# Optimization experiments

Hardware: AMD Instinct MI355X
Metric: run time of the kernel (lower is better)

The kernel has to match this reference:

```python
import jax, jax.numpy as jnp
import numpy as np

B, SEG, DIM = 8, 16, 1024  # H = W = D = SEG is forced by the Linear(dim, dim) on H*S etc.
HID = DIM // 4


def setup_inputs() -> dict:
    key = jax.random.key(0)
    ks = jax.random.split(key, 16)
    def lin(k, i, o):
        return jax.random.normal(k, (i, o), jnp.float32) * 0.02
    return {
        "x": jax.random.normal(ks[0], (B, SEG, SEG, SEG, DIM), jnp.float32),
        "wh": lin(ks[1], DIM, DIM), "bh": jnp.zeros((DIM,), jnp.float32),
        "ww": lin(ks[2], DIM, DIM), "bw": jnp.zeros((DIM,), jnp.float32),
        "wd": lin(ks[3], DIM, DIM), "bd": jnp.zeros((DIM,), jnp.float32),
        "wc": lin(ks[4], DIM, DIM), "bc": jnp.zeros((DIM,), jnp.float32),
        "w1": lin(ks[5], DIM, HID), "b1": jnp.zeros((HID,), jnp.float32),
        "w2": lin(ks[6], HID, 4 * DIM), "b2": jnp.zeros((4 * DIM,), jnp.float32),
        "wp": lin(ks[7], DIM, DIM), "bp": jnp.zeros((DIM,), jnp.float32),
    }


def reference(x, wh, bh, ww, bw, wd, bd, wc, bc, w1, b1, w2, b2, wp, bp):
    Bn, H, Wn, D, C = x.shape
    seg = SEG
    S = C // seg
    xr = x.reshape(Bn, H, Wn, D, seg, S)

    # h-branch: mix along H axis (H*S == C)
    h = xr.transpose(0, 4, 2, 3, 1, 5).reshape(Bn, seg, Wn, D, H * S)
    h = (h @ wh + bh).reshape(Bn, seg, Wn, D, H, S).transpose(0, 4, 2, 3, 1, 5).reshape(Bn, H, Wn, D, C)

    # w-branch: mix along W axis
    w = xr.transpose(0, 1, 4, 3, 2, 5).reshape(Bn, H, seg, D, Wn * S)
    w = (w @ ww + bw).reshape(Bn, H, seg, D, Wn, S).transpose(0, 1, 4, 3, 2, 5).reshape(Bn, H, Wn, D, C)

    # d-branch: mix along D axis
    d = xr.transpose(0, 1, 2, 4, 3, 5).reshape(Bn, H, Wn, seg, D * S)
    d = (d @ wd + bd).reshape(Bn, H, Wn, seg, D, S).transpose(0, 1, 2, 4, 3, 5).reshape(Bn, H, Wn, D, C)

    # c-branch: plain channel mixing
    c = x @ wc + bc

    # reweight gate: global-average-pool then small MLP -> softmax over the 4 branches
    a = (h + w + d + c).mean(axis=(1, 2, 3))                 # (B, C)
    a = jax.nn.gelu(a @ w1 + b1, approximate=False) @ w2 + b2  # (B, 4C)
    a = jax.nn.softmax(a.reshape(Bn, C, 4).transpose(2, 0, 1), axis=0)  # (4, B, C)
    a = a[:, :, None, None, None, :]                          # (4, B, 1, 1, 1, C)

    out = h * a[0] + w * a[1] + d * a[2] + c * a[3]
    return out @ wp + bp
```

## Files before the change

### kernel.cpp

```cpp
#include <hip/hip_runtime.h>
#include <cstdint>
#include <cstddef>

typedef unsigned short u16;
typedef __attribute__((ext_vector_type(8))) __bf16 bf16x8;
typedef __attribute__((ext_vector_type(4))) float f32x4;
typedef __attribute__((ext_vector_type(4))) unsigned int u32x4;

__device__ __forceinline__ float bf2f(u16 u){
  union { unsigned int i; float f; } x; x.i = ((unsigned int)u) << 16; return x.f;
}
__device__ __forceinline__ u16 f2bf(float f){
  union { float f; unsigned int i; } x; x.f = f;
  unsigned int i = x.i;
  return (u16)((i + 0x7fffu + ((i >> 16) & 1u)) >> 16);
}
__device__ __forceinline__ void load_lds16(const u16* g, u16* l){
  __builtin_amdgcn_global_load_lds((const __attribute__((address_space(1))) void*)g,
                                   (__attribute__((address_space(3))) void*)l, 16, 0, 0);
}

__global__ __launch_bounds__(256) void k_transpose(
    const float* __restrict__ wh, const float* __restrict__ ww,
    const float* __restrict__ wd, const float* __restrict__ wc,
    const float* __restrict__ wp, u16* __restrict__ wT)
{
  __shared__ u16 tile[32][33];
  const float* src = (blockIdx.z==0)?wh:(blockIdx.z==1)?ww:(blockIdx.z==2)?wd:(blockIdx.z==3)?wc:wp;
  u16* dst = wT + (size_t)blockIdx.z * 1048576;
  int x = blockIdx.x*32 + threadIdx.x;
  int y0 = blockIdx.y*32;
  for (int i = threadIdx.y; i < 32; i += 8)
    tile[i][threadIdx.x] = f2bf(src[(size_t)(y0+i)*1024 + x]);
  __syncthreads();
  int x2 = y0 + threadIdx.x;
  int y2 = blockIdx.x*32;
  for (int i = threadIdx.y; i < 32; i += 8)
    dst[(size_t)(y2+i)*1024 + x2] = tile[threadIdx.x][i];
}

__global__ __launch_bounds__(256) void k_psum(
    const float* __restrict__ x, u16* __restrict__ xbf, float* __restrict__ P_h,
    float* __restrict__ PwP, float* __restrict__ PdP)
{
  const int b = blockIdx.x, cs = blockIdx.y, hg = blockIdx.z;
  const int th = threadIdx.x >> 7, tc = threadIdx.x & 127;
  const int h = hg*2 + th, c = cs*128 + tc;
  const size_t base = ((size_t)b<<22) + ((size_t)h<<18) + c;
  const float* xb = x + base;
  u16* xo = xbf + base;
  float sh = 0.f;
  float aW[16] = {}, aD[16] = {};
#pragma unroll
  for (int w = 0; w < 16; ++w)
#pragma unroll
    for (int d = 0; d < 16; ++d){
      float v = xb[(w<<14) + (d<<10)];
      xo[(w<<14) + (d<<10)] = f2bf(v);
      sh += v; aW[w] += v; aD[d] += v;
    }
  P_h[(size_t)((b<<4)+h)*1024 + c] = sh;
  const int part = hg*2 + th;
  float* pw = PwP + ((size_t)part<<17) + ((size_t)b<<14) + c;
  float* pd = PdP + ((size_t)part<<17) + ((size_t)b<<14) + c;
#pragma unroll
  for (int w = 0; w < 16; ++w) pw[w<<10] = aW[w];
#pragma unroll
  for (int d = 0; d < 16; ++d) pd[d<<10] = aD[d];
}

__global__ __launch_bounds__(256) void k_psum2(
    const float* __restrict__ PwP, const float* __restrict__ PdP,
    float* __restrict__ P_w, float* __restrict__ P_d)
{
  int idx = blockIdx.x*256 + threadIdx.x;
  float s = 0.f, t = 0.f;
#pragma unroll
  for (int p = 0; p < 16; ++p){ s += PwP[(size_t)p*131072 + idx]; t += PdP[(size_t)p*131072 + idx]; }
  P_w[idx] = s; P_d[idx] = t;
}

__global__ __launch_bounds__(256) void k_wred(
    const float* __restrict__ wh, const float* __restrict__ ww, const float* __restrict__ wd,
    float* __restrict__ wred)
{
  const float* src = (blockIdx.y==0)?wh:(blockIdx.y==1)?ww:wd;
  int idx = blockIdx.x*256 + threadIdx.x;
  int k = idx >> 6, S = idx & 63;
  float s = 0.f;
#pragma unroll
  for (int i = 0; i < 16; ++i) s += src[(size_t)k*1024 + i*64 + S];
  wred[(size_t)blockIdx.y*65536 + idx] = s;
}

__global__ __launch_bounds__(256) void k_asum(
    const float* __restrict__ P_h, const float* __restrict__ P_w, const float* __restrict__ P_d,
    const float* __restrict__ wred, const float* __restrict__ wc,
    const float* __restrict__ bhv, const float* __restrict__ bwv,
    const float* __restrict__ bdv, const float* __restrict__ bcv,
    float* __restrict__ a_sum)
{
  const int b = blockIdx.x, cs = blockIdx.y, tid = threadIdx.x;
  const int tc = tid & 127, ti = tid >> 7;
  const int c = cs*128 + tc, sg = c >> 6, S = c & 63;
  __shared__ float xbar[1024];
  __shared__ float red[2][128];
  for (int k = tid; k < 1024; k += 256){
    float s = 0.f;
#pragma unroll
    for (int hh = 0; hh < 16; ++hh) s += P_h[(size_t)(b*16+hh)*1024 + k];
    xbar[k] = s;
  }
  __syncthreads();
  const float* Ph = P_h + (size_t)b*16384;
  const float* Pw = P_w + (size_t)b*16384;
  const float* Pd = P_d + (size_t)b*16384;
  const float* whr = wred, *wwr = wred + 65536, *wdr = wred + 131072;
  float acc = 0.f;
  for (int i = ti*8; i < ti*8 + 8; ++i){
#pragma unroll 8
    for (int si = 0; si < 64; ++si){
      int k = i*64 + si;
      acc += Ph[i*1024 + sg*64 + si] * whr[(size_t)k*64 + S]
           + Pw[i*1024 + sg*64 + si] * wwr[(size_t)k*64 + S]
           + Pd[i*1024 + sg*64 + si] * wdr[(size_t)k*64 + S];
    }
  }
#pragma unroll 8
  for (int k = ti*512; k < ti*512 + 512; ++k) acc += xbar[k] * wc[(size_t)k*1024 + c];
  red[ti][tc] = acc;
  __syncthreads();
  if (ti == 0){
    float bs = 0.f;
#pragma unroll
    for (int i = 0; i < 16; ++i) bs += bhv[i*64+S] + bwv[i*64+S] + bdv[i*64+S];
    a_sum[b*1024 + c] = red[0][tc] + red[1][tc] + 4096.f*bcv[c] + 256.f*bs;
  }
}

__global__ __launch_bounds__(256) void k_mlp1(
    const float* __restrict__ a_sum, const float* __restrict__ w1,
    const float* __restrict__ b1, float* __restrict__ z1g)
{
  const int b = blockIdx.x, tid = threadIdx.x;
  __shared__ float af[1024];
  for (int i = tid; i < 1024; i += 256) af[i] = a_sum[b*1024 + i] * (1.0f/4096.0f);
  __syncthreads();
  float acc = b1[tid];
#pragma unroll 8
  for (int k = 0; k < 1024; ++k) acc += af[k] * w1[(size_t)k*256 + tid];
  z1g[b*256 + tid] = 0.5f * acc * (1.0f + erff(acc * 0.70710678118654752f));
}

__global__ __launch_bounds__(128) void k_mlp2(
    const float* __restrict__ z1g, const float* __restrict__ w2,
    const float* __restrict__ b2, float* __restrict__ alpha)
{
  const int b = blockIdx.x, js = blockIdx.y, tid = threadIdx.x;
  __shared__ float z1[256];
  z1[tid] = z1g[b*256 + tid];
  z1[tid+128] = z1g[b*256 + tid + 128];
  __syncthreads();
  const int cch = js*128 + tid;
  const int j0 = cch*4;
  f32x4 acc = *(const f32x4*)(b2 + j0);
#pragma unroll 8
  for (int k = 0; k < 256; ++k){
    f32x4 wv4 = *(const f32x4*)(w2 + (size_t)k*4096 + j0);
    float z = z1[k];
    acc[0] += z*wv4[0]; acc[1] += z*wv4[1]; acc[2] += z*wv4[2]; acc[3] += z*wv4[3];
  }
  float m = fmaxf(fmaxf(acc[0], acc[1]), fmaxf(acc[2], acc[3]));
  float e0 = expf(acc[0]-m), e1 = expf(acc[1]-m), e2 = expf(acc[2]-m), e3 = expf(acc[3]-m);
  float inv = 1.0f / (e0+e1+e2+e3);
  alpha[0*8192 + b*1024 + cch] = e0*inv;
  alpha[1*8192 + b*1024 + cch] = e1*inv;
  alpha[2*8192 + b*1024 + cch] = e2*inv;
  alpha[3*8192 + b*1024 + cch] = e3*inv;
}


#define STAGE_A(buf, kk, kt) \
  load_lds16(gA0 + (size_t)(kt)*strideK + (kk)*32, sA + (buf)*16384 + (kk)*8192); \
  load_lds16(gA1 + (size_t)(kt)*strideK + (kk)*32, sA + (buf)*16384 + (kk)*8192 + 4096)
#define STAGE_B(buf, kk, kt) \
  load_lds16(gB0 + (kt)*64 + (kk)*32, sB + (buf)*16384 + (kk)*8192); \
  load_lds16(gB1 + (kt)*64 + (kk)*32, sB + (buf)*16384 + (kk)*8192 + 4096)

#define PHASE(h, kk, buf, STAGE_STMT, VM) do{ \
  const u16* ar_ = ldsA + (buf)*16384 + (kk)*8192 + ardoff + (h)*2048; \
  const u16* br_ = ldsB + (buf)*16384 + (kk)*8192 + brdoff; \
  bf16x8 af_[4], bf_[4]; \
  _Pragma("unroll") for (int m_ = 0; m_ < 4; ++m_) af_[m_] = *(const bf16x8*)(ar_ + m_*512); \
  _Pragma("unroll") for (int n_ = 0; n_ < 4; ++n_) bf_[n_] = *(const bf16x8*)(br_ + n_*512); \
  STAGE_STMT; \
  if (VM) asm volatile("s_waitcnt vmcnt(4)" ::: "memory"); \
  __builtin_amdgcn_s_barrier(); \
  asm volatile("s_waitcnt lgkmcnt(0)" ::: "memory"); \
  __builtin_amdgcn_sched_barrier(0); \
  __builtin_amdgcn_s_setprio(1); \
  _Pragma("unroll") for (int m_ = 0; m_ < 4; ++m_) \
    _Pragma("unroll") for (int n_ = 0; n_ < 4; ++n_) \
      acc[(h)*4+m_][n_] = __builtin_amdgcn_mfma_f32_16x16x32_bf16(af_[m_], bf_[n_], acc[(h)*4+m_][n_], 0, 0, 0); \
  __builtin_amdgcn_s_setprio(0); \
  __builtin_amdgcn_s_barrier(); \
}while(0)

#define GEMM_PROLOGUE() do{ \
  load_lds16(gA0, sA);                 load_lds16(gA1, sA + 4096); \
  load_lds16(gB0, sB);                 load_lds16(gB1, sB + 4096); \
  load_lds16(gA0 + 32, sA + 8192);     load_lds16(gA1 + 32, sA + 8192 + 4096); \
  load_lds16(gB0 + 32, sB + 8192);     load_lds16(gB1 + 32, sB + 8192 + 4096); \
  load_lds16(gA0 + strideK, sA + 16384);   load_lds16(gA1 + strideK, sA + 16384 + 4096); \
  load_lds16(gB0 + 64, sB + 16384);        load_lds16(gB1 + 64, sB + 16384 + 4096); \
  asm volatile("s_waitcnt vmcnt(4)" ::: "memory"); \
  __builtin_amdgcn_s_barrier(); \
}while(0)

#define GEMM_MAINLOOP() \
  for (int i = 0; i < 8; ++i){ \
    const int t1 = 2*i + 1; \
    const int t2 = (2*i + 2 < 16) ? 2*i + 2 : 15; \
    const int t3 = (2*i + 3 < 16) ? 2*i + 3 : 15; \
    PHASE(0,0,0, STAGE_A(1,1,t1), 0); \
    PHASE(1,0,0, STAGE_B(1,1,t1), 0); \
    PHASE(0,1,0, STAGE_A(0,0,t2), 0); \
    PHASE(1,1,0, STAGE_B(0,0,t2), 1); \
    PHASE(0,0,1, STAGE_A(0,1,t2), 0); \
    PHASE(1,0,1, STAGE_B(0,1,t2), 0); \
    PHASE(0,1,1, STAGE_A(1,0,t3), 0); \
    PHASE(1,1,1, STAGE_B(1,0,t3), 1); \
  }

__global__ __launch_bounds__(512, 2) void k_branch_gemm(
    const u16* __restrict__ xbf, const u16* __restrict__ wT,
    const float* __restrict__ bh, const float* __restrict__ bw,
    const float* __restrict__ bd, const float* __restrict__ bc,
    u16* __restrict__ hbuf, u16* __restrict__ wbuf,
    u16* __restrict__ dbuf, u16* __restrict__ cbuf)
{
  const int p = blockIdx.x;
  const int id = (p & 7) * 256 + (p >> 3);
  const int ntile  = id & 3;
  const int rtile  = (id >> 2) & 127;
  const int branch = id >> 9;

  const int tid = threadIdx.x;
  const int wv = tid >> 6, l = tid & 63;

  __shared__ __align__(16) u16 ldsA[32768];
  __shared__ __align__(16) u16 ldsB[32768];

  const u16* wsel = wT + (size_t)branch * 1048576;
  const float* bias = (branch==0)?bh:(branch==1)?bw:(branch==2)?bd:bc;
  u16* obuf         = (branch==0)?hbuf:(branch==1)?wbuf:(branch==2)?dbuf:cbuf;

  const int lr = l >> 2;
  const int qg = (l & 3) * 8;
  int strideK;
  size_t cb0, cb1;
  {
    const int q1 = rtile & 15, b_ = rtile >> 4;
    const size_t q2a = wv, q2b = wv + 8;
    if (branch == 0){
      cb0 = ((size_t)b_<<22) + (q2a<<14) + ((size_t)q1<<6);
      cb1 = ((size_t)b_<<22) + (q2b<<14) + ((size_t)q1<<6);
      strideK = 262144;
    } else if (branch == 1){
      cb0 = ((size_t)b_<<22) + ((size_t)q1<<18) + (q2a<<6);
      cb1 = ((size_t)b_<<22) + ((size_t)q1<<18) + (q2b<<6);
      strideK = 16384;
    } else if (branch == 2){
      cb0 = ((size_t)b_<<22) + ((size_t)q1<<18) + (q2a<<14);
      cb1 = ((size_t)b_<<22) + ((size_t)q1<<18) + (q2b<<14);
      strideK = 1024;
    } else {
      size_t r0 = (size_t)(rtile*256 + wv*16);
      cb0 = r0 << 10; cb1 = (r0 + 128) << 10;
      strideK = 64;
    }
  }
  const int rsh = (branch == 2) ? 6 : 10;
  const u16* gA0 = xbf + cb0 + ((size_t)lr << rsh) + qg;
  const u16* gA1 = xbf + cb1 + ((size_t)lr << rsh) + qg;
  const u16* gB0 = wsel + (size_t)(ntile*256 + wv*16 + lr) * 1024 + qg;
  const u16* gB1 = gB0 + 128*1024;
  u16* sA = ldsA + wv*512;
  u16* sB = ldsB + wv*512;

  const int wm = wv >> 2, wn = wv & 3;
  const int fr = l & 15;
  const int ardoff = (wm*128 + fr)*32 + (l >> 4)*8;
  const int brdoff = (wn*64  + fr)*32 + (l >> 4)*8;
  f32x4 acc[8][4] = {};

  GEMM_PROLOGUE();
  GEMM_MAINLOOP();

#pragma unroll
  for (int mg = 0; mg < 8; ++mg)
#pragma unroll
    for (int nf = 0; nf < 4; ++nf){
      int col = ntile*256 + wn*64 + nf*16 + fr;
      float bv = bias[col];
      int row0 = rtile*256 + wm*128 + mg*16 + (l>>4)*4;
#pragma unroll
      for (int rg = 0; rg < 4; ++rg)
        obuf[(size_t)(row0+rg)*1024 + col] = f2bf(acc[mg][nf][rg] + bv);
    }
}

__global__ __launch_bounds__(256) void k_mix(
    const u16* __restrict__ hbuf, const u16* __restrict__ wbuf,
    const u16* __restrict__ dbuf, const u16* __restrict__ cbuf,
    u16* __restrict__ mix, const float* __restrict__ alpha)
{
  int idx = blockIdx.x*256 + threadIdx.x;
  int p  = idx >> 7;
  int c0 = (idx & 127) << 3;
  int b = p >> 12, h = (p >> 8) & 15, w = (p >> 4) & 15, d = p & 15;
  int sg = c0 >> 6, s = c0 & 63;
  size_t bb = (size_t)b << 22;
  union { u32x4 v; u16 u[8]; } hv, wv, dv, cv, mv;
  hv.v = *(const u32x4*)(hbuf + bb + (sg<<18) + (w<<14) + (d<<10) + (h<<6) + s);
  wv.v = *(const u32x4*)(wbuf + bb + (h<<18) + (sg<<14) + (d<<10) + (w<<6) + s);
  dv.v = *(const u32x4*)(dbuf + bb + (h<<18) + (w<<14) + (sg<<10) + (d<<6) + s);
  cv.v = *(const u32x4*)(cbuf + ((size_t)p<<10) + c0);
  union { f32x4 f[2]; float a[8]; } a0, a1, a2, a3;
  const float* ab = alpha + b*1024 + c0;
  a0.f[0] = *(const f32x4*)(ab);         a0.f[1] = *(const f32x4*)(ab + 4);
  a1.f[0] = *(const f32x4*)(ab + 8192);  a1.f[1] = *(const f32x4*)(ab + 8196);
  a2.f[0] = *(const f32x4*)(ab + 16384); a2.f[1] = *(const f32x4*)(ab + 16388);
  a3.f[0] = *(const f32x4*)(ab + 24576); a3.f[1] = *(const f32x4*)(ab + 24580);
#pragma unroll
  for (int e = 0; e < 8; ++e){
    float m = a0.a[e]*bf2f(hv.u[e]) + a1.a[e]*bf2f(wv.u[e])
            + a2.a[e]*bf2f(dv.u[e]) + a3.a[e]*bf2f(cv.u[e]);
    mv.u[e] = f2bf(m);
  }
  *(u32x4*)(mix + ((size_t)p<<10) + c0) = mv.v;
}

__global__ __launch_bounds__(512, 2) void k_final_gemm(
    const u16* __restrict__ A, const u16* __restrict__ wpT,
    const float* __restrict__ bp, float* __restrict__ out)
{
  const int p = blockIdx.x;
  const int id = (p & 7) * 64 + (p >> 3);
  const int ntile = id & 3;
  const int rtile = id >> 2;

  const int tid = threadIdx.x;
  const int wv = tid >> 6, l = tid & 63;

  __shared__ __align__(16) u16 ldsA[32768];
  __shared__ __align__(16) u16 ldsB[32768];

  const int lr = l >> 2;
  const int qg = (l & 3) * 8;
  const int strideK = 64;
  const size_t r0 = (size_t)(rtile*256 + wv*16);
  const u16* gA0 = A + (r0 << 10) + ((size_t)lr << 10) + qg;
  const u16* gA1 = A + ((r0 + 128) << 10) + ((size_t)lr << 10) + qg;
  const u16* gB0 = wpT + (size_t)(ntile*256 + wv*16 + lr) * 1024 + qg;
  const u16* gB1 = gB0 + 128*1024;
  u16* sA = ldsA + wv*512;
  u16* sB = ldsB + wv*512;

  const int wm = wv >> 2, wn = wv & 3;
  const int fr = l & 15;
  const int ardoff = (wm*128 + fr)*32 + (l >> 4)*8;
  const int brdoff = (wn*64  + fr)*32 + (l >> 4)*8;
  f32x4 acc[8][4] = {};

  GEMM_PROLOGUE();
  GEMM_MAINLOOP();

#pragma unroll
  for (int mg = 0; mg < 8; ++mg)
#pragma unroll
    for (int nf = 0; nf < 4; ++nf){
      int col = ntile*256 + wn*64 + nf*16 + fr;
      float bv = bp[col];
      int row0 = rtile*256 + wm*128 + mg*16 + (l>>4)*4;
#pragma unroll
      for (int rg = 0; rg < 4; ++rg)
        out[(size_t)(row0+rg)*1024 + col] = acc[mg][nf][rg] + bv;
    }
}

extern "C" void kernel_launch(void* const* d_in, const int* in_sizes, int n_in,
                              void* d_out, int out_size, void* d_ws, size_t ws_size,
                              hipStream_t stream)
{
  const float* x  = (const float*)d_in[0];
  const float* wh = (const float*)d_in[1];
  const float* bh = (const float*)d_in[2];
  const float* ww = (const float*)d_in[3];
  const float* bw = (const float*)d_in[4];
  const float* wd = (const float*)d_in[5];
  const float* bd = (const float*)d_in[6];
  const float* wc = (const float*)d_in[7];
  const float* bc = (const float*)d_in[8];
  const float* w1 = (const float*)d_in[9];
  const float* b1 = (const float*)d_in[10];
  const float* w2 = (const float*)d_in[11];
  const float* b2 = (const float*)d_in[12];
  const float* wp = (const float*)d_in[13];
  const float* bp = (const float*)d_in[14];
  char* ws = (char*)d_ws;
  char* ob = (char*)d_out;

  u16*   xbf   = (u16*)(ws);
  u16*   hbuf  = (u16*)(ws + 67108864);
  u16*   wbuf  = (u16*)(ws + 134217728);
  u16*   wT    = (u16*)(ws + 201326592);
  float* a_sum = (float*)(ws + 211812352);
  float* alpha = (float*)(ws + 211845120);
  float* z1g   = (float*)(ws + 211976192);
  u16*   mixb  = xbf;

  float* PwP  = (float*)(ob);
  float* PdP  = (float*)(ob + 8388608);
  float* P_h  = (float*)(ob + 16777216);
  float* P_w  = (float*)(ob + 17301504);
  float* P_d  = (float*)(ob + 17825792);
  float* wred = (float*)(ob + 18350080);
  u16*   cbuf = (u16*)ob;
  u16*   dbuf = (u16*)(ob + 67108864);
  float* outp = (float*)d_out;

  k_transpose  <<<dim3(32, 32, 5), dim3(32, 8), 0, stream>>>(wh, ww, wd, wc, wp, wT);
  k_psum       <<<dim3(8, 8, 8),   256, 0, stream>>>(x, xbf, P_h, PwP, PdP);
  k_psum2      <<<dim3(512),       256, 0, stream>>>(PwP, PdP, P_w, P_d);
  k_wred       <<<dim3(256, 3),    256, 0, stream>>>(wh, ww, wd, wred);
  k_asum       <<<dim3(8, 8),      256, 0, stream>>>(P_h, P_w, P_d, wred, wc, bh, bw, bd, bc, a_sum);
  k_mlp1       <<<dim3(8),         256, 0, stream>>>(a_sum, w1, b1, z1g);
  k_mlp2       <<<dim3(8, 8),      128, 0, stream>>>(z1g, w2, b2, alpha);
  k_branch_gemm<<<dim3(2048),      512, 0, stream>>>(xbf, wT, bh, bw, bd, bc,
                                                     hbuf, wbuf, dbuf, cbuf);
  k_mix        <<<dim3(16384),     256, 0, stream>>>(hbuf, wbuf, dbuf, cbuf, mixb, alpha);
  k_final_gemm <<<dim3(512),       512, 0, stream>>>(mixb, wT + 4*1048576, bp, outp);
  (void)in_sizes; (void)n_in; (void)out_size; (void)ws_size;
}
```

Measured before the change: 968.8 us.

## Swizzle LDS tile layout and write branch outputs in natural order

Applies an XOR swizzle to the K-chunk index for both global-to-LDS loads and the MFMA fragment reads in both GEMM kernels, to cut LDS bank conflicts. The branch GEMM epilogue now scatters each result straight back into the original (B,H,W,D,C) layout. This lets the mix kernel read all four branch buffers with the same contiguous offset instead of gathering them through per-branch transposed addresses. The epilogue stores become strided per branch, which may reduce write coalescing.

```diff
diff --git a/kernel.cpp b/kernel.cpp
--- a/kernel.cpp
+++ b/kernel.cpp
@@ -256,7 +256,7 @@
   u16* obuf         = (branch==0)?hbuf:(branch==1)?wbuf:(branch==2)?dbuf:cbuf;
 
   const int lr = l >> 2;
-  const int qg = (l & 3) * 8;
+  const int qg = ((l & 3) ^ ((lr >> 1) & 3)) * 8;
   int strideK;
   size_t cb0, cb1;
   {
@@ -290,24 +290,37 @@
 
   const int wm = wv >> 2, wn = wv & 3;
   const int fr = l & 15;
-  const int ardoff = (wm*128 + fr)*32 + (l >> 4)*8;
-  const int brdoff = (wn*64  + fr)*32 + (l >> 4)*8;
+  const int cswz = ((l >> 4) ^ ((fr >> 1) & 3)) * 8;
+  const int ardoff = (wm*128 + fr)*32 + cswz;
+  const int brdoff = (wn*64  + fr)*32 + cswz;
   f32x4 acc[8][4] = {};
 
   GEMM_PROLOGUE();
   GEMM_MAINLOOP();
 
-#pragma unroll
-  for (int mg = 0; mg < 8; ++mg)
+  const int bb_ = rtile >> 4, p1 = rtile & 15;
+  int sc, s1, s2, s3;
+  if      (branch==0){ sc=18; s1=6;  s2=14; s3=10; }
+  else if (branch==1){ sc=14; s1=18; s2=6;  s3=10; }
+  else if (branch==2){ sc=10; s1=18; s2=14; s3=6;  }
+  else               { sc=6;  s1=18; s2=14; s3=10; }
+#pragma unroll
+  for (int mg = 0; mg < 8; ++mg){
+    const int p2 = wm*8 + mg;
 #pragma unroll
     for (int nf = 0; nf < 4; ++nf){
       int col = ntile*256 + wn*64 + nf*16 + fr;
+      int ch = col >> 6, cl = col & 63;
       float bv = bias[col];
-      int row0 = rtile*256 + wm*128 + mg*16 + (l>>4)*4;
-#pragma unroll
-      for (int rg = 0; rg < 4; ++rg)
-        obuf[(size_t)(row0+rg)*1024 + col] = f2bf(acc[mg][nf][rg] + bv);
+      size_t base = ((size_t)bb_<<22) | ((size_t)p1<<s1) | ((size_t)ch<<sc)
+                  | ((size_t)p2<<s2) | (size_t)cl;
+#pragma unroll
+      for (int rg = 0; rg < 4; ++rg){
+        int p3 = (l>>4)*4 + rg;
+        obuf[base + ((size_t)p3<<s3)] = f2bf(acc[mg][nf][rg] + bv);
+      }
     }
+  }
 }
 
 __global__ __launch_bounds__(256) void k_mix(
@@ -318,14 +331,13 @@
   int idx = blockIdx.x*256 + threadIdx.x;
   int p  = idx >> 7;
   int c0 = (idx & 127) << 3;
-  int b = p >> 12, h = (p >> 8) & 15, w = (p >> 4) & 15, d = p & 15;
-  int sg = c0 >> 6, s = c0 & 63;
-  size_t bb = (size_t)b << 22;
+  int b = p >> 12;
+  size_t off = ((size_t)p << 10) + c0;
   union { u32x4 v; u16 u[8]; } hv, wv, dv, cv, mv;
-  hv.v = *(const u32x4*)(hbuf + bb + (sg<<18) + (w<<14) + (d<<10) + (h<<6) + s);
-  wv.v = *(const u32x4*)(wbuf + bb + (h<<18) + (sg<<14) + (d<<10) + (w<<6) + s);
-  dv.v = *(const u32x4*)(dbuf + bb + (h<<18) + (w<<14) + (sg<<10) + (d<<6) + s);
-  cv.v = *(const u32x4*)(cbuf + ((size_t)p<<10) + c0);
+  hv.v = *(const u32x4*)(hbuf + off);
+  wv.v = *(const u32x4*)(wbuf + off);
+  dv.v = *(const u32x4*)(dbuf + off);
+  cv.v = *(const u32x4*)(cbuf + off);
   union { f32x4 f[2]; float a[8]; } a0, a1, a2, a3;
   const float* ab = alpha + b*1024 + c0;
   a0.f[0] = *(const f32x4*)(ab);         a0.f[1] = *(const f32x4*)(ab + 4);
@@ -338,7 +350,7 @@
             + a2.a[e]*bf2f(dv.u[e]) + a3.a[e]*bf2f(cv.u[e]);
     mv.u[e] = f2bf(m);
   }
-  *(u32x4*)(mix + ((size_t)p<<10) + c0) = mv.v;
+  *(u32x4*)(mix + off) = mv.v;
 }
 
 __global__ __launch_bounds__(512, 2) void k_final_gemm(
@@ -357,7 +369,7 @@
   __shared__ __align__(16) u16 ldsB[32768];
 
   const int lr = l >> 2;
-  const int qg = (l & 3) * 8;
+  const int qg = ((l & 3) ^ ((lr >> 1) & 3)) * 8;
   const int strideK = 64;
   const size_t r0 = (size_t)(rtile*256 + wv*16);
   const u16* gA0 = A + (r0 << 10) + ((size_t)lr << 10) + qg;
@@ -369,8 +381,9 @@
 
   const int wm = wv >> 2, wn = wv & 3;
   const int fr = l & 15;
-  const int ardoff = (wm*128 + fr)*32 + (l >> 4)*8;
-  const int brdoff = (wn*64  + fr)*32 + (l >> 4)*8;
+  const int cswz = ((l >> 4) ^ ((fr >> 1) & 3)) * 8;
+  const int ardoff = (wm*128 + fr)*32 + cswz;
+  const int brdoff = (wn*64  + fr)*32 + cswz;
   f32x4 acc[8][4] = {};
 
   GEMM_PROLOGUE();
```

New measurement: 938.9 us. 1.03x faster.
